# Performance work log

Hardware: AMD Instinct MI355X
Metric: run time of the kernel (lower is better)

## Reference

```python
import jax, jax.numpy as jnp
import numpy as np

D_LINK = 64   # link_state_dim
D_PATH = 64   # path_state_dim
T = 3
MAX_LEN = 8   # max hops per path (max(seqs)+1)
R_UNITS = 256


def _glorot(k, shape):
    lim = np.sqrt(6.0 / (shape[0] + shape[-1])).astype(np.float32)
    return jax.random.uniform(k, shape, minval=-lim, maxval=lim, dtype=jnp.float32)


def setup_inputs() -> dict:
    key = jax.random.key(0)
    ks = jax.random.split(key, 16)
    n_links, n_paths, L = 50000, 100000, MAX_LEN
    capacities = jax.random.uniform(ks[0], (n_links,), dtype=jnp.float32) + 0.5
    traffic = jax.random.uniform(ks[1], (n_paths,), dtype=jnp.float32)
    # every path traverses L links; entries sorted by path id (tf.segment_sum assumption)
    paths = jnp.repeat(jnp.arange(n_paths, dtype=jnp.int32), L)
    seqs = jnp.tile(jnp.arange(L, dtype=jnp.int32), n_paths)
    links = jax.random.randint(ks[2], (n_paths * L,), 0, n_links, dtype=jnp.int32)
    return dict(
        capacities=capacities, traffic=traffic, links=links, paths=paths, seqs=seqs,
        Wx_p=_glorot(ks[3], (D_LINK, 3 * D_PATH)), Wh_p=_glorot(ks[4], (D_PATH, 3 * D_PATH)),
        b_p=jnp.zeros((3 * D_PATH,), jnp.float32),
        Wx_e=_glorot(ks[5], (D_PATH, 3 * D_LINK)), Wh_e=_glorot(ks[6], (D_LINK, 3 * D_LINK)),
        b_e=jnp.zeros((3 * D_LINK,), jnp.float32),
        W_r1=_glorot(ks[7], (D_PATH, R_UNITS)), b_r1=jnp.zeros((R_UNITS,), jnp.float32),
        W_r2=_glorot(ks[8], (R_UNITS, R_UNITS)), b_r2=jnp.zeros((R_UNITS,), jnp.float32),
        W_f=_glorot(ks[9], (D_PATH + R_UNITS, 1)), b_f=jnp.zeros((1,), jnp.float32),
        n_links=n_links, n_paths=n_paths,
    )


def gru_cell(x, h, Wx, Wh, b):
    # Keras GRUCell (reset_after=False), gate order z, r, h
    gx = x @ Wx + b
    gh = h @ Wh
    u = h.shape[-1]
    z = jax.nn.sigmoid(gx[..., :u] + gh[..., :u])
    r = jax.nn.sigmoid(gx[..., u:2 * u] + gh[..., u:2 * u])
    hc = jnp.tanh(gx[..., 2 * u:] + r * gh[..., 2 * u:])
    return z * h + (1.0 - z) * hc


def routenet_fwd(capacities, traffic, links, paths, seqs,
                 Wx_p, Wh_p, b_p, Wx_e, Wh_e, b_e,
                 W_r1, b_r1, W_r2, b_r2, W_f, b_f, n_links, n_paths):
    link_state = jnp.concatenate(
        [capacities[:, None], jnp.zeros((n_links, D_LINK - 1), capacities.dtype)], axis=1)
    path_state = jnp.concatenate(
        [traffic[:, None], jnp.zeros((n_paths, D_PATH - 1), traffic.dtype)], axis=1)
    lens = jax.ops.segment_sum(jnp.ones_like(paths), paths, num_segments=n_paths)  # [P]

    for _ in range(T):
        h_ = link_state[links]                                        # [E, D_LINK]
        link_inputs = jnp.zeros((n_paths, MAX_LEN, D_LINK), h_.dtype).at[paths, seqs].set(h_)

        def step(h, inp):
            xt, t = inp
            hn = gru_cell(xt, h, Wx_p, Wh_p, b_p)
            valid = (t < lens)[:, None]
            hn = jnp.where(valid, hn, h)          # dynamic_rnn copies state past seq len
            out = jnp.where(valid, hn, 0.0)       # and emits zeros there
            return hn, out

        path_state, outs = jax.lax.scan(
            step, path_state,
            (jnp.transpose(link_inputs, (1, 0, 2)), jnp.arange(MAX_LEN)))
        m = jnp.transpose(outs, (1, 0, 2))[paths, seqs]               # [E, D_PATH]
        m = jax.ops.segment_sum(m, links, num_segments=n_links)      # [n_links, D_PATH]
        link_state = gru_cell(m, link_state, Wx_e, Wh_e, b_e)

    r = jax.nn.selu(path_state @ W_r1 + b_r1)
    r = jax.nn.selu(r @ W_r2 + b_r2)          # dropout inactive (training=False)
    o = jnp.concatenate([r, path_state], axis=1) @ W_f + b_f
    return o


def reference(capacities, traffic, links, paths, seqs,
              Wx_p, Wh_p, b_p, Wx_e, Wh_e, b_e,
              W_r1, b_r1, W_r2, b_r2, W_f, b_f, n_links, n_paths):
    return routenet_fwd(capacities, traffic, links, paths, seqs,
                        Wx_p, Wh_p, b_p, Wx_e, Wh_e, b_e,
                        W_r1, b_r1, W_r2, b_r2, W_f, b_f, n_links, n_paths)
```

## Files before the change

kernel.cpp:

```cpp
#include <hip/hip_runtime.h>

typedef unsigned short ushort_t;
typedef unsigned int   uint_t;
typedef short bf16x8 __attribute__((ext_vector_type(8)));
typedef float f32x4  __attribute__((ext_vector_type(4)));

#define MFMA16(a,b,c) __builtin_amdgcn_mfma_f32_16x16x32_bf16((a),(b),(c),0,0,0)

static __device__ __forceinline__ float bf2f(ushort_t b) {
  union { uint_t u; float f; } v; v.u = ((uint_t)b) << 16; return v.f;
}
static __device__ __forceinline__ ushort_t f2bf(float f) {
  union { float f; uint_t u; } v; v.f = f;
  uint_t r = v.u + 0x7fffu + ((v.u >> 16) & 1u);
  return (ushort_t)(r >> 16);
}
static __device__ __forceinline__ float frcp(float x) { return __builtin_amdgcn_rcpf(x); }
static __device__ __forceinline__ float sigm(float x) { return frcp(1.0f + __expf(-x)); }
static __device__ __forceinline__ float ftanh(float x) { return 1.0f - 2.0f * frcp(1.0f + __expf(2.0f * x)); }
static __device__ __forceinline__ float selu_f(float x) {
  float e = 1.6732632423543772f * (__expf(x) - 1.0f);
  return 1.0507009873554805f * (x > 0.0f ? x : e);
}
static __device__ __forceinline__ bf16x8 pack8(float4 a, float4 b) {
  bf16x8 r;
  r[0] = (short)f2bf(a.x); r[1] = (short)f2bf(a.y); r[2] = (short)f2bf(a.z); r[3] = (short)f2bf(a.w);
  r[4] = (short)f2bf(b.x); r[5] = (short)f2bf(b.y); r[6] = (short)f2bf(b.z); r[7] = (short)f2bf(b.w);
  return r;
}
static __device__ __forceinline__ void split8(float4 a, float4 b, bf16x8& hi, bf16x8& lo) {
  hi = pack8(a, b);
  float4 ra, rb;
  ra.x = a.x - bf2f((ushort_t)hi[0]); ra.y = a.y - bf2f((ushort_t)hi[1]);
  ra.z = a.z - bf2f((ushort_t)hi[2]); ra.w = a.w - bf2f((ushort_t)hi[3]);
  rb.x = b.x - bf2f((ushort_t)hi[4]); rb.y = b.y - bf2f((ushort_t)hi[5]);
  rb.z = b.z - bf2f((ushort_t)hi[6]); rb.w = b.w - bf2f((ushort_t)hi[7]);
  lo = pack8(ra, rb);
}

#define GFRAG(ptr, f) (*(const bf16x8*)&(ptr)[(((f) * 64 + lane)) * 8])
#define LFRAG(arr, f) (*(const bf16x8*)&(arr)[(((f) * 64 + lane)) * 8])

__global__ void detect_dtype(const uint_t* __restrict__ caps, int* __restrict__ flag) {
  int lane = threadIdx.x;
  uint_t d = caps[lane];
  uint_t lo = d & 0xFFFFu, hi = d >> 16;
  bool isbf = (lo >= 0x3F00u && lo <= 0x3FC0u) && (hi >= 0x3F00u && hi <= 0x3FC0u);
  unsigned long long m = __ballot(isbf);
  if (lane == 0) *flag = (__popcll(m) >= 48) ? 1 : 0;
}

#define NARR 14
struct ConvDesc {
  const void* src[NARR];
  float*      dst[NARR];
  int         n[NARR];
  int         blk0[NARR + 1];
};
__global__ void conv_all(ConvDesc d, const int* __restrict__ flag) {
  int isbf = *flag;
  int b = blockIdx.x;
  int a = 0;
  while (a + 1 < NARR && b >= d.blk0[a + 1]) ++a;
  int idx = (b - d.blk0[a]) * 256 + threadIdx.x;
  if (idx >= d.n[a]) return;
  d.dst[a][idx] = isbf ? bf2f(((const ushort_t*)d.src[a])[idx])
                       : ((const float*)d.src[a])[idx];
}

struct PackAll {
  const float* A[8];
  const float* B[8];
  ushort_t* dH[8];
  ushort_t* dL[8];
  int srcN[8], colOff[8], splitK[8], nCk[8], NT[8], blk0[9];
};
__global__ void pack_all(PackAll P) {
  int b = blockIdx.x;
  int a = 0;
  while (a + 1 < 8 && b >= P.blk0[a + 1]) ++a;
  int i = (b - P.blk0[a]) * 256 + threadIdx.x;
  int j = i & 7;
  int lane = (i >> 3) & 63;
  int f = i >> 9;
  int c = f / P.NT[a], nt = f - c * P.NT[a];
  int k = c * 32 + ((lane >> 4) << 3) + j;
  int n = P.colOff[a] + nt * 16 + (lane & 15);
  float v = (k < P.splitK[a]) ? P.A[a][k * P.srcN[a] + n]
                              : P.B[a][(k - P.splitK[a]) * P.srcN[a] + n];
  ushort_t hi = f2bf(v);
  P.dH[a][i] = hi;
  P.dL[a][i] = f2bf(v - bf2f(hi));
}

__global__ void init_states(const float* __restrict__ caps, const float* __restrict__ traffic,
                            ushort_t* __restrict__ linkHL,
                            float* __restrict__ path_state, int n_links, int n_paths) {
  long i = (long)blockIdx.x * 256 + threadIdx.x;
  long total = (long)(n_links + n_paths) * 64;
  if (i >= total) return;
  int row = (int)(i >> 6), col = (int)(i & 63);
  if (row < n_links) {
    float v = (col == 0) ? caps[row] : 0.0f;
    ushort_t hi = f2bf(v);
    linkHL[(long)row * 128 + col] = hi;
    linkHL[(long)row * 128 + 64 + col] = f2bf(v - bf2f(hi));
  } else {
    int pr = row - n_links;
    path_state[(long)pr * 64 + col] = (col == 0) ? traffic[pr] : 0.0f;
  }
}

__global__ void hist_k(const int* __restrict__ links, int* __restrict__ cnt, int E) {
  int e = blockIdx.x * 256 + threadIdx.x;
  if (e < E) atomicAdd(&cnt[links[e]], 1);
}
__global__ void scan_k(const int* __restrict__ cnt, int* __restrict__ base,
                       int* __restrict__ cursor, int n) {
  __shared__ int part[256];
  int tid = threadIdx.x;
  int chunk = (n + 255) / 256;
  int lo = tid * chunk, hiEnd = lo + chunk; if (hiEnd > n) hiEnd = n;
  int s = 0;
  for (int i = lo; i < hiEnd; ++i) s += cnt[i];
  part[tid] = s;
  __syncthreads();
  if (tid == 0) { int acc = 0; for (int i = 0; i < 256; ++i) { int v = part[i]; part[i] = acc; acc += v; } }
  __syncthreads();
  int acc = part[tid];
  for (int i = lo; i < hiEnd; ++i) { base[i] = acc; cursor[i] = acc; acc += cnt[i]; }
}
__global__ void fill_k(const int* __restrict__ links, int* __restrict__ cursor,
                       int* __restrict__ pos_of, int E) {
  int e = blockIdx.x * 256 + threadIdx.x;
  if (e >= E) return;
  pos_of[e] = atomicAdd(&cursor[links[e]], 1);
}

__global__ __launch_bounds__(256) void agg_kernel(
    const ushort_t* __restrict__ mH,
    const int* __restrict__ base, const int* __restrict__ cnt,
    float* __restrict__ agg, int n_links) {
  int l = blockIdx.x * 4 + (threadIdx.x >> 6);
  if (l >= n_links) return;
  int lane = threadIdx.x & 63;
  int s = base[l], d = cnt[l];
  float acc = 0.0f;
  for (int i = 0; i < d; ++i) acc += bf2f(mH[(long)(s + i) * 64 + lane]);
  agg[(long)l * 64 + lane] = acc;
}

#define PWB 7
__global__ __launch_bounds__(448) void path_kernel_bf16(
    const int* __restrict__ links,
    const ushort_t* __restrict__ linkHL,
    float* __restrict__ path_state,
    ushort_t* __restrict__ mH, int mmode, int store_m,
    const int* __restrict__ pos_of, float* __restrict__ agg,
    const ushort_t* __restrict__ wzrH, const ushort_t* __restrict__ wcH,
    const float* __restrict__ bp, const int* __restrict__ flagp, int n_paths) {
  __shared__ __align__(16) ushort_t s_wzr[32 * 512];
  __shared__ __align__(16) ushort_t s_wc[16 * 512];
  __shared__ __align__(16) ushort_t s_hh[PWB][16][68];
  __shared__ __align__(16) ushort_t s_hl[PWB][16][68];
  __shared__ float s_bias[192];

  if (flagp[0] == 0) return;

  int tid = threadIdx.x;
  {
    uint_t* s0 = (uint_t*)s_wzr; const uint_t* g0 = (const uint_t*)wzrH;
    for (int i = tid; i < 8192; i += 448) s0[i] = g0[i];
    uint_t* s1 = (uint_t*)s_wc;  const uint_t* g1 = (const uint_t*)wcH;
    for (int i = tid; i < 4096; i += 448) s1[i] = g1[i];
    for (int i = tid; i < 192; i += 448) s_bias[i] = bp[i];
  }

  int wv = tid >> 6, lane = tid & 63, l15 = lane & 15, quad = lane >> 4;
  int p0 = (blockIdx.x * PWB + wv) * 16;
  bool valid = (p0 < n_paths);

  float h[4][4];
  if (valid) {
#pragma unroll
    for (int tt = 0; tt < 4; ++tt)
#pragma unroll
      for (int r = 0; r < 4; ++r) {
        float v = path_state[(long)(p0 + quad * 4 + r) * 64 + tt * 16 + l15];
        h[tt][r] = v;
        ushort_t hi = f2bf(v);
        s_hh[wv][quad * 4 + r][tt * 16 + l15] = hi;
        s_hl[wv][quad * 4 + r][tt * 16 + l15] = f2bf(v - bf2f(hi));
      }
  }
  __syncthreads();
  if (!valid) return;

  for (int t = 0; t < 8; ++t) {
    int la = links[(p0 + l15) * 8 + t];
    const ushort_t* xr = linkHL + (long)la * 128;
    bf16x8 axH0 = *(const bf16x8*)(xr + quad * 8);
    bf16x8 axH1 = *(const bf16x8*)(xr + 32 + quad * 8);
    bf16x8 axL0 = *(const bf16x8*)(xr + 64 + quad * 8);
    bf16x8 axL1 = *(const bf16x8*)(xr + 96 + quad * 8);
    bf16x8 ahH0 = *(const bf16x8*)&s_hh[wv][l15][quad * 8];
    bf16x8 ahH1 = *(const bf16x8*)&s_hh[wv][l15][32 + quad * 8];
    bf16x8 ahL0 = *(const bf16x8*)&s_hl[wv][l15][quad * 8];
    bf16x8 ahL1 = *(const bf16x8*)&s_hl[wv][l15][32 + quad * 8];

    f32x4 azr[8];
#pragma unroll
    for (int nt = 0; nt < 8; ++nt) {
      f32x4 acc = {0.f, 0.f, 0.f, 0.f};
      acc = MFMA16(axH0, LFRAG(s_wzr, nt), acc);
      acc = MFMA16(axH1, LFRAG(s_wzr, 8 + nt), acc);
      acc = MFMA16(ahH0, LFRAG(s_wzr, 16 + nt), acc);
      acc = MFMA16(ahH1, LFRAG(s_wzr, 24 + nt), acc);
      acc = MFMA16(axL0, LFRAG(s_wzr, nt), acc);
      acc = MFMA16(axL1, LFRAG(s_wzr, 8 + nt), acc);
      acc = MFMA16(ahL0, LFRAG(s_wzr, 16 + nt), acc);
      acc = MFMA16(ahL1, LFRAG(s_wzr, 24 + nt), acc);
      azr[nt] = acc;
    }
    f32x4 axc[4], ahc[4];
#pragma unroll
    for (int nt = 0; nt < 4; ++nt) {
      f32x4 a = {0.f, 0.f, 0.f, 0.f};
      a = MFMA16(axH0, LFRAG(s_wc, nt), a);
      a = MFMA16(axH1, LFRAG(s_wc, 4 + nt), a);
      a = MFMA16(axL0, LFRAG(s_wc, nt), a);
      a = MFMA16(axL1, LFRAG(s_wc, 4 + nt), a);
      axc[nt] = a;
      f32x4 b = {0.f, 0.f, 0.f, 0.f};
      b = MFMA16(ahH0, LFRAG(s_wc, 8 + nt), b);
      b = MFMA16(ahH1, LFRAG(s_wc, 12 + nt), b);
      b = MFMA16(ahL0, LFRAG(s_wc, 8 + nt), b);
      b = MFMA16(ahL1, LFRAG(s_wc, 12 + nt), b);
      ahc[nt] = b;
    }

    int pr[4] = {0, 0, 0, 0};
    if (store_m) {
      if (mmode == 2) {
#pragma unroll
        for (int r = 0; r < 4; ++r) pr[r] = links[(p0 + quad * 4 + r) * 8 + t];
      } else {
#pragma unroll
        for (int r = 0; r < 4; ++r) pr[r] = pos_of[(p0 + quad * 4 + r) * 8 + t];
      }
    }

#pragma unroll
    for (int tt = 0; tt < 4; ++tt) {
      int col = tt * 16 + l15;
      float bz = s_bias[col], br = s_bias[64 + col], bc = s_bias[128 + col];
#pragma unroll
      for (int r = 0; r < 4; ++r) {
        float z   = sigm(azr[tt][r] + bz);
        float rr  = sigm(azr[4 + tt][r] + br);
        float hcv = ftanh(axc[tt][r] + bc + rr * ahc[tt][r]);
        float hn  = z * h[tt][r] + (1.0f - z) * hcv;
        h[tt][r] = hn;
        if (store_m) {
          if (mmode == 1) mH[(long)pr[r] * 64 + col] = f2bf(hn);
          else atomicAdd(&agg[(long)pr[r] * 64 + col], hn);
        }
        ushort_t hi = f2bf(hn);
        s_hh[wv][quad * 4 + r][col] = hi;
        s_hl[wv][quad * 4 + r][col] = f2bf(hn - bf2f(hi));
      }
    }
  }

#pragma unroll
  for (int tt = 0; tt < 4; ++tt)
#pragma unroll
    for (int r = 0; r < 4; ++r)
      path_state[(long)(p0 + quad * 4 + r) * 64 + tt * 16 + l15] = h[tt][r];
}

#define PW 13
__global__ __launch_bounds__(832) void path_kernel_f32(
    const int* __restrict__ links,
    const ushort_t* __restrict__ linkHL,
    float* __restrict__ path_state,
    ushort_t* __restrict__ mH, int mmode, int store_m,
    const int* __restrict__ pos_of, float* __restrict__ agg,
    const ushort_t* __restrict__ wzrH, const ushort_t* __restrict__ wzrL,
    const ushort_t* __restrict__ wcH,  const ushort_t* __restrict__ wcL,
    const float* __restrict__ bp, const int* __restrict__ flagp,
    int n_paths, int nGroups) {
  __shared__ __align__(16) ushort_t s_wzr[2][32 * 512];
  __shared__ __align__(16) ushort_t s_wc[2][16 * 512];
  __shared__ __align__(16) ushort_t s_hh[PW][16][72];
  __shared__ __align__(16) ushort_t s_hl[PW][16][72];
  __shared__ float s_bias[192];

  if (flagp[0] != 0) return;

  int tid = threadIdx.x;
  {
    uint_t* s0 = (uint_t*)s_wzr[0]; const uint_t* g0 = (const uint_t*)wzrH;
    for (int i = tid; i < 8192; i += 832) s0[i] = g0[i];
    uint_t* s1 = (uint_t*)s_wc[0];  const uint_t* g1 = (const uint_t*)wcH;
    for (int i = tid; i < 4096; i += 832) s1[i] = g1[i];
    uint_t* s2 = (uint_t*)s_wzr[1]; const uint_t* g2 = (const uint_t*)wzrL;
    for (int i = tid; i < 8192; i += 832) s2[i] = g2[i];
    uint_t* s3 = (uint_t*)s_wc[1];  const uint_t* g3 = (const uint_t*)wcL;
    for (int i = tid; i < 4096; i += 832) s3[i] = g3[i];
    for (int i = tid; i < 192; i += 832) s_bias[i] = bp[i];
  }
  __syncthreads();

  int wv = tid >> 6, lane = tid & 63, l15 = lane & 15, quad = lane >> 4;

  for (int g = 0; g < nGroups; ++g) {
    int slot = g * gridDim.x + blockIdx.x;
    int p0 = (slot * PW + wv) * 16;
    if (p0 >= n_paths) continue;

    float h[4][4];
#pragma unroll
    for (int tt = 0; tt < 4; ++tt)
#pragma unroll
      for (int r = 0; r < 4; ++r) {
        float v = path_state[(long)(p0 + quad * 4 + r) * 64 + tt * 16 + l15];
        h[tt][r] = v;
        ushort_t hi = f2bf(v);
        s_hh[wv][quad * 4 + r][tt * 16 + l15] = hi;
        s_hl[wv][quad * 4 + r][tt * 16 + l15] = f2bf(v - bf2f(hi));
      }

    const int* lrow = links + (long)(p0 + l15) * 8;
    {
      int la0 = lrow[0];
      const ushort_t* x0 = linkHL + (long)la0 * 128;
      bf16x8 nH0 = *(const bf16x8*)(x0 + quad * 8);
      bf16x8 nH1 = *(const bf16x8*)(x0 + 32 + quad * 8);
      bf16x8 nL0 = *(const bf16x8*)(x0 + 64 + quad * 8);
      bf16x8 nL1 = *(const bf16x8*)(x0 + 96 + quad * 8);

      for (int t = 0; t < 8; ++t) {
        bf16x8 axH0 = nH0, axH1 = nH1, axL0 = nL0, axL1 = nL1;
        if (t < 7) {
          int la2 = lrow[t + 1];
          const ushort_t* x2 = linkHL + (long)la2 * 128;
          nH0 = *(const bf16x8*)(x2 + quad * 8);
          nH1 = *(const bf16x8*)(x2 + 32 + quad * 8);
          nL0 = *(const bf16x8*)(x2 + 64 + quad * 8);
          nL1 = *(const bf16x8*)(x2 + 96 + quad * 8);
        }
        int pr[4] = {0, 0, 0, 0};
        if (store_m) {
          if (mmode == 2) {
#pragma unroll
            for (int r = 0; r < 4; ++r) pr[r] = links[(long)(p0 + quad * 4 + r) * 8 + t];
          } else {
#pragma unroll
            for (int r = 0; r < 4; ++r) pr[r] = pos_of[(long)(p0 + quad * 4 + r) * 8 + t];
          }
        }
        bf16x8 ahH0 = *(const bf16x8*)&s_hh[wv][l15][quad * 8];
        bf16x8 ahH1 = *(const bf16x8*)&s_hh[wv][l15][32 + quad * 8];
        bf16x8 ahL0 = *(const bf16x8*)&s_hl[wv][l15][quad * 8];
        bf16x8 ahL1 = *(const bf16x8*)&s_hl[wv][l15][32 + quad * 8];

        f32x4 azr[8];
#pragma unroll
        for (int nt = 0; nt < 8; ++nt) {
          f32x4 acc = {0.f, 0.f, 0.f, 0.f};
          acc = MFMA16(axH0, LFRAG(s_wzr[0], nt), acc);
          acc = MFMA16(axH1, LFRAG(s_wzr[0], 8 + nt), acc);
          acc = MFMA16(axL0, LFRAG(s_wzr[0], nt), acc);
          acc = MFMA16(axL1, LFRAG(s_wzr[0], 8 + nt), acc);
          acc = MFMA16(axH0, LFRAG(s_wzr[1], nt), acc);
          acc = MFMA16(axH1, LFRAG(s_wzr[1], 8 + nt), acc);
          acc = MFMA16(ahH0, LFRAG(s_wzr[0], 16 + nt), acc);
          acc = MFMA16(ahH1, LFRAG(s_wzr[0], 24 + nt), acc);
          acc = MFMA16(ahL0, LFRAG(s_wzr[0], 16 + nt), acc);
          acc = MFMA16(ahL1, LFRAG(s_wzr[0], 24 + nt), acc);
          acc = MFMA16(ahH0, LFRAG(s_wzr[1], 16 + nt), acc);
          acc = MFMA16(ahH1, LFRAG(s_wzr[1], 24 + nt), acc);
          azr[nt] = acc;
        }
        f32x4 axc[4], ahc[4];
#pragma unroll
        for (int nt = 0; nt < 4; ++nt) {
          f32x4 a = {0.f, 0.f, 0.f, 0.f};
          a = MFMA16(axH0, LFRAG(s_wc[0], nt), a);
          a = MFMA16(axH1, LFRAG(s_wc[0], 4 + nt), a);
          a = MFMA16(axL0, LFRAG(s_wc[0], nt), a);
          a = MFMA16(axL1, LFRAG(s_wc[0], 4 + nt), a);
          a = MFMA16(axH0, LFRAG(s_wc[1], nt), a);
          a = MFMA16(axH1, LFRAG(s_wc[1], 4 + nt), a);
          axc[nt] = a;
          f32x4 b = {0.f, 0.f, 0.f, 0.f};
          b = MFMA16(ahH0, LFRAG(s_wc[0], 8 + nt), b);
          b = MFMA16(ahH1, LFRAG(s_wc[0], 12 + nt), b);
          b = MFMA16(ahL0, LFRAG(s_wc[0], 8 + nt), b);
          b = MFMA16(ahL1, LFRAG(s_wc[0], 12 + nt), b);
          b = MFMA16(ahH0, LFRAG(s_wc[1], 8 + nt), b);
          b = MFMA16(ahH1, LFRAG(s_wc[1], 12 + nt), b);
          ahc[nt] = b;
        }

#pragma unroll
        for (int tt = 0; tt < 4; ++tt) {
          int col = tt * 16 + l15;
          float bz = s_bias[col], br = s_bias[64 + col], bc = s_bias[128 + col];
#pragma unroll
          for (int r = 0; r < 4; ++r) {
            float z   = sigm(azr[tt][r] + bz);
            float rr  = sigm(azr[4 + tt][r] + br);
            float hcv = ftanh(axc[tt][r] + bc + rr * ahc[tt][r]);
            float hn  = z * h[tt][r] + (1.0f - z) * hcv;
            h[tt][r] = hn;
            if (store_m) {
              if (mmode == 1) mH[(long)pr[r] * 64 + col] = f2bf(hn);
              else atomicAdd(&agg[(long)pr[r] * 64 + col], hn);
            }
            ushort_t hi = f2bf(hn);
            s_hh[wv][quad * 4 + r][col] = hi;
            s_hl[wv][quad * 4 + r][col] = f2bf(hn - bf2f(hi));
          }
        }
      }
    }

#pragma unroll
    for (int tt = 0; tt < 4; ++tt)
#pragma unroll
      for (int r = 0; r < 4; ++r)
        path_state[(long)(p0 + quad * 4 + r) * 64 + tt * 16 + l15] = h[tt][r];
  }
}

__global__ __launch_bounds__(320) void link_kernel(
    const float* __restrict__ agg,
    ushort_t* __restrict__ linkHL,
    const ushort_t* __restrict__ wzrH, const ushort_t* __restrict__ wzrL,
    const ushort_t* __restrict__ wcH,  const ushort_t* __restrict__ wcL,
    const float* __restrict__ be, const int* __restrict__ flagp) {
  __shared__ __align__(16) ushort_t s_wzr[2][32 * 512];
  __shared__ __align__(16) ushort_t s_wc[2][16 * 512];
  __shared__ float s_bias[192];

  int tid = threadIdx.x;
  int wlo = (flagp[0] == 0) ? 1 : 0;
  {
    uint_t* s0 = (uint_t*)s_wzr[0]; const uint_t* g0 = (const uint_t*)wzrH;
    for (int i = tid; i < 8192; i += 320) s0[i] = g0[i];
    uint_t* s1 = (uint_t*)s_wc[0];  const uint_t* g1 = (const uint_t*)wcH;
    for (int i = tid; i < 4096; i += 320) s1[i] = g1[i];
    if (wlo) {
      uint_t* s2 = (uint_t*)s_wzr[1]; const uint_t* g2 = (const uint_t*)wzrL;
      for (int i = tid; i < 8192; i += 320) s2[i] = g2[i];
      uint_t* s3 = (uint_t*)s_wc[1];  const uint_t* g3 = (const uint_t*)wcL;
      for (int i = tid; i < 4096; i += 320) s3[i] = g3[i];
    }
    for (int i = tid; i < 192; i += 320) s_bias[i] = be[i];
  }
  __syncthreads();

  int wv = tid >> 6, lane = tid & 63, l15 = lane & 15, quad = lane >> 4;
  int l0 = (blockIdx.x * 5 + wv) * 16;

  const float* arow = agg + (long)(l0 + l15) * 64;
  float4 f0 = *(const float4*)(arow + quad * 8);
  float4 f1 = *(const float4*)(arow + quad * 8 + 4);
  float4 f2 = *(const float4*)(arow + 32 + quad * 8);
  float4 f3 = *(const float4*)(arow + 36 + quad * 8);
  bf16x8 axH0, axL0, axH1, axL1;
  split8(f0, f1, axH0, axL0);
  split8(f2, f3, axH1, axL1);
  const ushort_t* hr = linkHL + (long)(l0 + l15) * 128;
  bf16x8 ahH0 = *(const bf16x8*)(hr + quad * 8);
  bf16x8 ahH1 = *(const bf16x8*)(hr + 32 + quad * 8);
  bf16x8 ahL0 = *(const bf16x8*)(hr + 64 + quad * 8);
  bf16x8 ahL1 = *(const bf16x8*)(hr + 96 + quad * 8);

  float h[4][4];
#pragma unroll
  for (int tt = 0; tt < 4; ++tt)
#pragma unroll
    for (int r = 0; r < 4; ++r) {
      long row = (long)(l0 + quad * 4 + r) * 128;
      int col = tt * 16 + l15;
      h[tt][r] = bf2f(linkHL[row + col]) + bf2f(linkHL[row + 64 + col]);
    }

  f32x4 azr[8];
#pragma unroll
  for (int nt = 0; nt < 8; ++nt) {
    f32x4 acc = {0.f, 0.f, 0.f, 0.f};
    acc = MFMA16(axH0, LFRAG(s_wzr[0], nt), acc);
    acc = MFMA16(axH1, LFRAG(s_wzr[0], 8 + nt), acc);
    acc = MFMA16(ahH0, LFRAG(s_wzr[0], 16 + nt), acc);
    acc = MFMA16(ahH1, LFRAG(s_wzr[0], 24 + nt), acc);
    acc = MFMA16(axL0, LFRAG(s_wzr[0], nt), acc);
    acc = MFMA16(axL1, LFRAG(s_wzr[0], 8 + nt), acc);
    acc = MFMA16(ahL0, LFRAG(s_wzr[0], 16 + nt), acc);
    acc = MFMA16(ahL1, LFRAG(s_wzr[0], 24 + nt), acc);
    azr[nt] = acc;
  }
  f32x4 axc[4], ahc[4];
#pragma unroll
  for (int nt = 0; nt < 4; ++nt) {
    f32x4 a = {0.f, 0.f, 0.f, 0.f};
    a = MFMA16(axH0, LFRAG(s_wc[0], nt), a);
    a = MFMA16(axH1, LFRAG(s_wc[0], 4 + nt), a);
    a = MFMA16(axL0, LFRAG(s_wc[0], nt), a);
    a = MFMA16(axL1, LFRAG(s_wc[0], 4 + nt), a);
    axc[nt] = a;
    f32x4 b = {0.f, 0.f, 0.f, 0.f};
    b = MFMA16(ahH0, LFRAG(s_wc[0], 8 + nt), b);
    b = MFMA16(ahH1, LFRAG(s_wc[0], 12 + nt), b);
    b = MFMA16(ahL0, LFRAG(s_wc[0], 8 + nt), b);
    b = MFMA16(ahL1, LFRAG(s_wc[0], 12 + nt), b);
    ahc[nt] = b;
  }
  if (wlo) {
#pragma unroll
    for (int nt = 0; nt < 8; ++nt) {
      azr[nt] = MFMA16(axH0, LFRAG(s_wzr[1], nt), azr[nt]);
      azr[nt] = MFMA16(axH1, LFRAG(s_wzr[1], 8 + nt), azr[nt]);
      azr[nt] = MFMA16(ahH0, LFRAG(s_wzr[1], 16 + nt), azr[nt]);
      azr[nt] = MFMA16(ahH1, LFRAG(s_wzr[1], 24 + nt), azr[nt]);
    }
#pragma unroll
    for (int nt = 0; nt < 4; ++nt) {
      axc[nt] = MFMA16(axH0, LFRAG(s_wc[1], nt), axc[nt]);
      axc[nt] = MFMA16(axH1, LFRAG(s_wc[1], 4 + nt), axc[nt]);
      ahc[nt] = MFMA16(ahH0, LFRAG(s_wc[1], 8 + nt), ahc[nt]);
      ahc[nt] = MFMA16(ahH1, LFRAG(s_wc[1], 12 + nt), ahc[nt]);
    }
  }

#pragma unroll
  for (int tt = 0; tt < 4; ++tt) {
    int col = tt * 16 + l15;
    float bz = s_bias[col], br = s_bias[64 + col], bc = s_bias[128 + col];
#pragma unroll
    for (int r = 0; r < 4; ++r) {
      float z   = sigm(azr[tt][r] + bz);
      float rr  = sigm(azr[4 + tt][r] + br);
      float hcv = ftanh(axc[tt][r] + bc + rr * ahc[tt][r]);
      float hn  = z * h[tt][r] + (1.0f - z) * hcv;
      long row = (long)(l0 + quad * 4 + r) * 128;
      ushort_t hi = f2bf(hn);
      linkHL[row + col] = hi;
      linkHL[row + 64 + col] = f2bf(hn - bf2f(hi));
    }
  }
}

#define RW 8
__global__ __launch_bounds__(512) void readout_kernel(
    const float* __restrict__ path_state, int n_paths,
    const ushort_t* __restrict__ wr1H, const ushort_t* __restrict__ wr1L,
    const ushort_t* __restrict__ wr2H, const ushort_t* __restrict__ wr2L,
    const float* __restrict__ br1, const float* __restrict__ br2,
    const float* __restrict__ Wf, const float* __restrict__ bfp,
    void* __restrict__ outp, const int* __restrict__ flagp) {
  __shared__ __align__(16) ushort_t s_r1h[RW][16][264];
  __shared__ __align__(16) ushort_t s_r1l[RW][16][264];
  int tid = threadIdx.x;
  int wv = tid >> 6, lane = tid & 63, l15 = lane & 15, quad = lane >> 4;
  int p0 = (blockIdx.x * RW + wv) * 16;
  if (p0 >= n_paths) return;
  int isbf = flagp[0];
  int wlo = (isbf == 0) ? 1 : 0;

  const float* prow = path_state + (long)(p0 + l15) * 64;
  float4 g0 = *(const float4*)(prow + quad * 8);
  float4 g1 = *(const float4*)(prow + quad * 8 + 4);
  float4 g2 = *(const float4*)(prow + 32 + quad * 8);
  float4 g3 = *(const float4*)(prow + 36 + quad * 8);
  bf16x8 axH0, axL0, axH1, axL1;
  split8(g0, g1, axH0, axL0);
  split8(g2, g3, axH1, axL1);

  f32x4 a1[16];
#pragma unroll
  for (int nt = 0; nt < 16; ++nt) {
    f32x4 acc = {0.f, 0.f, 0.f, 0.f};
    acc = MFMA16(axH0, GFRAG(wr1H, nt), acc);
    acc = MFMA16(axH1, GFRAG(wr1H, 16 + nt), acc);
    acc = MFMA16(axL0, GFRAG(wr1H, nt), acc);
    acc = MFMA16(axL1, GFRAG(wr1H, 16 + nt), acc);
    a1[nt] = acc;
  }
  if (wlo) {
#pragma unroll
    for (int nt = 0; nt < 16; ++nt) {
      a1[nt] = MFMA16(axH0, GFRAG(wr1L, nt), a1[nt]);
      a1[nt] = MFMA16(axH1, GFRAG(wr1L, 16 + nt), a1[nt]);
    }
  }
#pragma unroll
  for (int tt = 0; tt < 16; ++tt) {
    float bb = br1[tt * 16 + l15];
#pragma unroll
    for (int r = 0; r < 4; ++r) {
      float v = selu_f(a1[tt][r] + bb);
      ushort_t hi = f2bf(v);
      s_r1h[wv][quad * 4 + r][tt * 16 + l15] = hi;
      s_r1l[wv][quad * 4 + r][tt * 16 + l15] = f2bf(v - bf2f(hi));
    }
  }

  f32x4 a2[16];
  f32x4 zero = {0.f, 0.f, 0.f, 0.f};
#pragma unroll
  for (int nt = 0; nt < 16; ++nt) a2[nt] = zero;
#pragma unroll
  for (int c = 0; c < 8; ++c) {
    bf16x8 afH = *(const bf16x8*)&s_r1h[wv][l15][c * 32 + quad * 8];
    bf16x8 afL = *(const bf16x8*)&s_r1l[wv][l15][c * 32 + quad * 8];
#pragma unroll
    for (int nt = 0; nt < 16; ++nt) {
      a2[nt] = MFMA16(afH, GFRAG(wr2H, c * 16 + nt), a2[nt]);
      a2[nt] = MFMA16(afL, GFRAG(wr2H, c * 16 + nt), a2[nt]);
    }
    if (wlo) {
#pragma unroll
      for (int nt = 0; nt < 16; ++nt)
        a2[nt] = MFMA16(afH, GFRAG(wr2L, c * 16 + nt), a2[nt]);
    }
  }

  float part[4] = {0.f, 0.f, 0.f, 0.f};
#pragma unroll
  for (int tt = 0; tt < 16; ++tt) {
    float wf = Wf[tt * 16 + l15];
    float bb = br2[tt * 16 + l15];
#pragma unroll
    for (int r = 0; r < 4; ++r) part[r] += selu_f(a2[tt][r] + bb) * wf;
  }
  float wfh0 = Wf[256 + l15 * 4 + 0];
  float wfh1 = Wf[256 + l15 * 4 + 1];
  float wfh2 = Wf[256 + l15 * 4 + 2];
  float wfh3 = Wf[256 + l15 * 4 + 3];
#pragma unroll
  for (int r = 0; r < 4; ++r) {
    const float4 hh = *(const float4*)&path_state[(long)(p0 + quad * 4 + r) * 64 + l15 * 4];
    part[r] += hh.x * wfh0 + hh.y * wfh1 + hh.z * wfh2 + hh.w * wfh3;
  }
#pragma unroll
  for (int msk = 1; msk < 16; msk <<= 1)
#pragma unroll
    for (int r = 0; r < 4; ++r) part[r] += __shfl_xor(part[r], msk, 64);
  if (l15 == 0) {
    float bfv = bfp[0];
    if (isbf) {
#pragma unroll
      for (int r = 0; r < 4; ++r) ((ushort_t*)outp)[p0 + quad * 4 + r] = f2bf(part[r] + bfv);
    } else {
#pragma unroll
      for (int r = 0; r < 4; ++r) ((float*)outp)[p0 + quad * 4 + r] = part[r] + bfv;
    }
  }
}

extern "C" void kernel_launch(void* const* d_in, const int* in_sizes, int n_in,
                              void* d_out, int out_size, void* d_ws, size_t ws_size,
                              hipStream_t stream) {
  const int n_links = in_sizes[0];
  const int n_paths = in_sizes[1];
  const int E       = in_sizes[2];

  char* w = (char*)d_ws;
  size_t off = 0;
  auto take = [&](size_t bytes) { size_t o = off; off += (bytes + 255) & ~(size_t)255; return o; };
  float*    path_state = (float*)(w + take((size_t)n_paths * 64 * 4));
  float*    agg        = (float*)(w + take((size_t)n_links * 64 * 4));
  ushort_t* linkHL     = (ushort_t*)(w + take((size_t)n_links * 128 * 2));
  int*      flag       = (int*)(w + take(256));
  ushort_t* wzrH_p = (ushort_t*)(w + take(32768));
  ushort_t* wzrL_p = (ushort_t*)(w + take(32768));
  ushort_t* wcH_p  = (ushort_t*)(w + take(16384));
  ushort_t* wcL_p  = (ushort_t*)(w + take(16384));
  ushort_t* wzrH_e = (ushort_t*)(w + take(32768));
  ushort_t* wzrL_e = (ushort_t*)(w + take(32768));
  ushort_t* wcH_e  = (ushort_t*)(w + take(16384));
  ushort_t* wcL_e  = (ushort_t*)(w + take(16384));
  ushort_t* wr1H   = (ushort_t*)(w + take(32768));
  ushort_t* wr1L   = (ushort_t*)(w + take(32768));
  ushort_t* wr2H   = (ushort_t*)(w + take(131072));
  ushort_t* wr2L   = (ushort_t*)(w + take(131072));
  float* c_caps    = (float*)(w + take((size_t)in_sizes[0] * 4));
  float* c_traffic = (float*)(w + take((size_t)in_sizes[1] * 4));
  float* c_Wx_p = (float*)(w + take((size_t)in_sizes[5] * 4));
  float* c_Wh_p = (float*)(w + take((size_t)in_sizes[6] * 4));
  float* c_b_p  = (float*)(w + take((size_t)in_sizes[7] * 4));
  float* c_Wx_e = (float*)(w + take((size_t)in_sizes[8] * 4));
  float* c_Wh_e = (float*)(w + take((size_t)in_sizes[9] * 4));
  float* c_b_e  = (float*)(w + take((size_t)in_sizes[10] * 4));
  float* c_Wr1  = (float*)(w + take((size_t)in_sizes[11] * 4));
  float* c_br1  = (float*)(w + take((size_t)in_sizes[12] * 4));
  float* c_Wr2  = (float*)(w + take((size_t)in_sizes[13] * 4));
  float* c_br2  = (float*)(w + take((size_t)in_sizes[14] * 4));
  float* c_Wf   = (float*)(w + take((size_t)in_sizes[15] * 4));
  float* c_bf   = (float*)(w + take((size_t)in_sizes[16] * 4));
  int* cnt    = (int*)(w + take((size_t)n_links * 4));
  int* base   = (int*)(w + take((size_t)n_links * 4));
  int* cursor = (int*)(w + take((size_t)n_links * 4));
  int* pos_of = (int*)(w + take((size_t)E * 4));

  size_t rem = (ws_size > off) ? (ws_size - off) : 0;
  int mmode;
  ushort_t* mH = nullptr;
  if (rem >= (size_t)E * 64 * 2 + 256) { mmode = 1; mH = (ushort_t*)(w + take((size_t)E * 64 * 2)); }
  else mmode = 2;

  detect_dtype<<<1, 64, 0, stream>>>((const uint_t*)d_in[0], flag);

  ConvDesc cd;
  float* dsts[NARR] = {c_caps, c_traffic, c_Wx_p, c_Wh_p, c_b_p, c_Wx_e, c_Wh_e, c_b_e,
                       c_Wr1, c_br1, c_Wr2, c_br2, c_Wf, c_bf};
  int    srcs[NARR] = {0, 1, 5, 6, 7, 8, 9, 10, 11, 12, 13, 14, 15, 16};
  int nblk = 0;
  for (int a = 0; a < NARR; ++a) {
    cd.src[a] = d_in[srcs[a]];
    cd.dst[a] = dsts[a];
    cd.n[a] = in_sizes[srcs[a]];
    cd.blk0[a] = nblk;
    nblk += (cd.n[a] + 255) / 256;
  }
  cd.blk0[NARR] = nblk;
  conv_all<<<nblk, 256, 0, stream>>>(cd, flag);

  {
    long total = (long)(n_links + n_paths) * 64;
    int blocks = (int)((total + 255) / 256);
    init_states<<<blocks, 256, 0, stream>>>(c_caps, c_traffic, linkHL, path_state,
                                            n_links, n_paths);
  }
  {
    PackAll P;
    const float* As[8] = {c_Wx_p, c_Wx_p, c_Wh_p, c_Wx_e, c_Wx_e, c_Wh_e, c_Wr1, c_Wr2};
    const float* Bs[8] = {c_Wh_p, c_Wx_p, c_Wh_p, c_Wh_e, c_Wx_e, c_Wh_e, c_Wr1, c_Wr2};
    ushort_t* dH[8] = {wzrH_p, wcH_p, wcH_p + 4096, wzrH_e, wcH_e, wcH_e + 4096, wr1H, wr2H};
    ushort_t* dL[8] = {wzrL_p, wcL_p, wcL_p + 4096, wzrL_e, wcL_e, wcL_e + 4096, wr1L, wr2L};
    int srcN[8]   = {192, 192, 192, 192, 192, 192, 256, 256};
    int colOff[8] = {0, 128, 128, 0, 128, 128, 0, 0};
    int splitK[8] = {64, 64, 64, 64, 64, 64, 64, 256};
    int nCk[8]    = {4, 2, 2, 4, 2, 2, 2, 8};
    int NT[8]     = {8, 4, 4, 8, 4, 4, 16, 16};
    int pb = 0;
    for (int a = 0; a < 8; ++a) {
      P.A[a] = As[a]; P.B[a] = Bs[a]; P.dH[a] = dH[a]; P.dL[a] = dL[a];
      P.srcN[a] = srcN[a]; P.colOff[a] = colOff[a]; P.splitK[a] = splitK[a];
      P.nCk[a] = nCk[a]; P.NT[a] = NT[a]; P.blk0[a] = pb;
      pb += nCk[a] * NT[a] * 2;
    }
    P.blk0[8] = pb;
    pack_all<<<pb, 256, 0, stream>>>(P);
  }

  const int* links = (const int*)d_in[2];
  if (mmode == 1) {
    (void)hipMemsetAsync(cnt, 0, (size_t)n_links * 4, stream);
    hist_k<<<(E + 255) / 256, 256, 0, stream>>>(links, cnt, E);
    scan_k<<<1, 256, 0, stream>>>(cnt, base, cursor, n_links);
    fill_k<<<(E + 255) / 256, 256, 0, stream>>>(links, cursor, pos_of, E);
  }

  int grid_bf = (n_paths + 16 * PWB - 1) / (16 * PWB);
  int slots   = (n_paths + 16 * PW - 1) / (16 * PW);
  int gridF   = slots < 256 ? slots : 256;
  int nGroups = (slots + gridF - 1) / gridF;

  for (int it = 0; it < 3; ++it) {
    int store_m = (it < 2) ? 1 : 0;
    if (mmode == 2 && store_m) (void)hipMemsetAsync(agg, 0, (size_t)n_links * 64 * 4, stream);
    path_kernel_bf16<<<grid_bf, 448, 0, stream>>>(
        links, linkHL, path_state, mH, mmode, store_m, pos_of, agg,
        wzrH_p, wcH_p, c_b_p, flag, n_paths);
    path_kernel_f32<<<gridF, 832, 0, stream>>>(
        links, linkHL, path_state, mH, mmode, store_m, pos_of, agg,
        wzrH_p, wzrL_p, wcH_p, wcL_p, c_b_p, flag, n_paths, nGroups);
    if (it < 2) {
      if (mmode == 1)
        agg_kernel<<<(n_links + 3) / 4, 256, 0, stream>>>(mH, base, cnt, agg, n_links);
      link_kernel<<<n_links / 80, 320, 0, stream>>>(agg, linkHL,
                                                    wzrH_e, wzrL_e, wcH_e, wcL_e, c_b_e, flag);
    }
  }
  readout_kernel<<<(n_paths + 16 * RW - 1) / (16 * RW), 512, 0, stream>>>(
      path_state, n_paths, wr1H, wr1L, wr2H, wr2L,
      c_br1, c_br2, c_Wf, c_bf, d_out, flag);
}
```

Measured before the change: 1.162 ms.

## Store path messages in fp32 when workspace allows; stage readout W2 in LDS

Adds a new message mode that keeps per-edge path outputs in fp32 instead of bf16 whenever the workspace is large enough, and the sorted gather aggregation reads those fp32 values. Separately, the readout kernel drops from 8 to 6 waves per block and copies W_r2 into shared memory one 32-row chunk at a time instead of reading MFMA fragments from global memory. The fp32 path doubles message write and read traffic but avoids bf16 rounding of messages. The readout staging adds block-wide barriers, and invalid waves now stay resident so they can join those barriers.

Measured after the change: 1.459 ms. +25.6%, slower.

```diff
diff --git a/kernel.cpp b/kernel.cpp
--- a/kernel.cpp
+++ b/kernel.cpp
@@ -138,7 +138,7 @@
 }
 
 __global__ __launch_bounds__(256) void agg_kernel(
-    const ushort_t* __restrict__ mH,
+    const float* __restrict__ mF, const ushort_t* __restrict__ mH, int mmode,
     const int* __restrict__ base, const int* __restrict__ cnt,
     float* __restrict__ agg, int n_links) {
   int l = blockIdx.x * 4 + (threadIdx.x >> 6);
@@ -146,7 +146,11 @@
   int lane = threadIdx.x & 63;
   int s = base[l], d = cnt[l];
   float acc = 0.0f;
-  for (int i = 0; i < d; ++i) acc += bf2f(mH[(long)(s + i) * 64 + lane]);
+  if (mmode == 0) {
+    for (int i = 0; i < d; ++i) acc += mF[(long)(s + i) * 64 + lane];
+  } else {
+    for (int i = 0; i < d; ++i) acc += bf2f(mH[(long)(s + i) * 64 + lane]);
+  }
   agg[(long)l * 64 + lane] = acc;
 }
 
@@ -155,7 +159,7 @@
     const int* __restrict__ links,
     const ushort_t* __restrict__ linkHL,
     float* __restrict__ path_state,
-    ushort_t* __restrict__ mH, int mmode, int store_m,
+    float* __restrict__ mF, ushort_t* __restrict__ mH, int mmode, int store_m,
     const int* __restrict__ pos_of, float* __restrict__ agg,
     const ushort_t* __restrict__ wzrH, const ushort_t* __restrict__ wcH,
     const float* __restrict__ bp, const int* __restrict__ flagp, int n_paths) {
@@ -262,7 +266,8 @@
         float hn  = z * h[tt][r] + (1.0f - z) * hcv;
         h[tt][r] = hn;
         if (store_m) {
-          if (mmode == 1) mH[(long)pr[r] * 64 + col] = f2bf(hn);
+          if (mmode == 0)      mF[(long)pr[r] * 64 + col] = hn;
+          else if (mmode == 1) mH[(long)pr[r] * 64 + col] = f2bf(hn);
           else atomicAdd(&agg[(long)pr[r] * 64 + col], hn);
         }
         ushort_t hi = f2bf(hn);
@@ -284,7 +289,7 @@
     const int* __restrict__ links,
     const ushort_t* __restrict__ linkHL,
     float* __restrict__ path_state,
-    ushort_t* __restrict__ mH, int mmode, int store_m,
+    float* __restrict__ mF, ushort_t* __restrict__ mH, int mmode, int store_m,
     const int* __restrict__ pos_of, float* __restrict__ agg,
     const ushort_t* __restrict__ wzrH, const ushort_t* __restrict__ wzrL,
     const ushort_t* __restrict__ wcH,  const ushort_t* __restrict__ wcL,
@@ -416,7 +421,8 @@
             float hn  = z * h[tt][r] + (1.0f - z) * hcv;
             h[tt][r] = hn;
             if (store_m) {
-              if (mmode == 1) mH[(long)pr[r] * 64 + col] = f2bf(hn);
+              if (mmode == 0)      mF[(long)pr[r] * 64 + col] = hn;
+              else if (mmode == 1) mH[(long)pr[r] * 64 + col] = f2bf(hn);
               else atomicAdd(&agg[(long)pr[r] * 64 + col], hn);
             }
             ushort_t hi = f2bf(hn);
@@ -554,8 +560,8 @@
   }
 }
 
-#define RW 8
-__global__ __launch_bounds__(512) void readout_kernel(
+#define RW 6
+__global__ __launch_bounds__(384) void readout_kernel(
     const float* __restrict__ path_state, int n_paths,
     const ushort_t* __restrict__ wr1H, const ushort_t* __restrict__ wr1L,
     const ushort_t* __restrict__ wr2H, const ushort_t* __restrict__ wr2L,
@@ -564,48 +570,52 @@
     void* __restrict__ outp, const int* __restrict__ flagp) {
   __shared__ __align__(16) ushort_t s_r1h[RW][16][264];
   __shared__ __align__(16) ushort_t s_r1l[RW][16][264];
+  __shared__ __align__(16) ushort_t s_w2h[16 * 512];
+  __shared__ __align__(16) ushort_t s_w2l[16 * 512];
   int tid = threadIdx.x;
   int wv = tid >> 6, lane = tid & 63, l15 = lane & 15, quad = lane >> 4;
   int p0 = (blockIdx.x * RW + wv) * 16;
-  if (p0 >= n_paths) return;
+  bool valid = (p0 < n_paths);
   int isbf = flagp[0];
   int wlo = (isbf == 0) ? 1 : 0;
 
-  const float* prow = path_state + (long)(p0 + l15) * 64;
-  float4 g0 = *(const float4*)(prow + quad * 8);
-  float4 g1 = *(const float4*)(prow + quad * 8 + 4);
-  float4 g2 = *(const float4*)(prow + 32 + quad * 8);
-  float4 g3 = *(const float4*)(prow + 36 + quad * 8);
   bf16x8 axH0, axL0, axH1, axL1;
-  split8(g0, g1, axH0, axL0);
-  split8(g2, g3, axH1, axL1);
-
   f32x4 a1[16];
-#pragma unroll
-  for (int nt = 0; nt < 16; ++nt) {
-    f32x4 acc = {0.f, 0.f, 0.f, 0.f};
-    acc = MFMA16(axH0, GFRAG(wr1H, nt), acc);
-    acc = MFMA16(axH1, GFRAG(wr1H, 16 + nt), acc);
-    acc = MFMA16(axL0, GFRAG(wr1H, nt), acc);
-    acc = MFMA16(axL1, GFRAG(wr1H, 16 + nt), acc);
-    a1[nt] = acc;
-  }
-  if (wlo) {
+  if (valid) {
+    const float* prow = path_state + (long)(p0 + l15) * 64;
+    float4 g0 = *(const float4*)(prow + quad * 8);
+    float4 g1 = *(const float4*)(prow + quad * 8 + 4);
+    float4 g2 = *(const float4*)(prow + 32 + quad * 8);
+    float4 g3 = *(const float4*)(prow + 36 + quad * 8);
+    split8(g0, g1, axH0, axL0);
+    split8(g2, g3, axH1, axL1);
+
 #pragma unroll
     for (int nt = 0; nt < 16; ++nt) {
-      a1[nt] = MFMA16(axH0, GFRAG(wr1L, nt), a1[nt]);
-      a1[nt] = MFMA16(axH1, GFRAG(wr1L, 16 + nt), a1[nt]);
-    }
-  }
-#pragma unroll
-  for (int tt = 0; tt < 16; ++tt) {
-    float bb = br1[tt * 16 + l15];
-#pragma unroll
-    for (int r = 0; r < 4; ++r) {
-      float v = selu_f(a1[tt][r] + bb);
-      ushort_t hi = f2bf(v);
-      s_r1h[wv][quad * 4 + r][tt * 16 + l15] = hi;
-      s_r1l[wv][quad * 4 + r][tt * 16 + l15] = f2bf(v - bf2f(hi));
+      f32x4 acc = {0.f, 0.f, 0.f, 0.f};
+      acc = MFMA16(axH0, GFRAG(wr1H, nt), acc);
+      acc = MFMA16(axH1, GFRAG(wr1H, 16 + nt), acc);
+      acc = MFMA16(axL0, GFRAG(wr1H, nt), acc);
+      acc = MFMA16(axL1, GFRAG(wr1H, 16 + nt), acc);
+      a1[nt] = acc;
+    }
+    if (wlo) {
+#pragma unroll
+      for (int nt = 0; nt < 16; ++nt) {
+        a1[nt] = MFMA16(axH0, GFRAG(wr1L, nt), a1[nt]);
+        a1[nt] = MFMA16(axH1, GFRAG(wr1L, 16 + nt), a1[nt]);
+      }
+    }
+#pragma unroll
+    for (int tt = 0; tt < 16; ++tt) {
+      float bb = br1[tt * 16 + l15];
+#pragma unroll
+      for (int r = 0; r < 4; ++r) {
+        float v = selu_f(a1[tt][r] + bb);
+        ushort_t hi = f2bf(v);
+        s_r1h[wv][quad * 4 + r][tt * 16 + l15] = hi;
+        s_r1l[wv][quad * 4 + r][tt * 16 + l15] = f2bf(v - bf2f(hi));
+      }
     }
   }
 
@@ -613,21 +623,34 @@
   f32x4 zero = {0.f, 0.f, 0.f, 0.f};
 #pragma unroll
   for (int nt = 0; nt < 16; ++nt) a2[nt] = zero;
-#pragma unroll
+
   for (int c = 0; c < 8; ++c) {
-    bf16x8 afH = *(const bf16x8*)&s_r1h[wv][l15][c * 32 + quad * 8];
-    bf16x8 afL = *(const bf16x8*)&s_r1l[wv][l15][c * 32 + quad * 8];
-#pragma unroll
-    for (int nt = 0; nt < 16; ++nt) {
-      a2[nt] = MFMA16(afH, GFRAG(wr2H, c * 16 + nt), a2[nt]);
-      a2[nt] = MFMA16(afL, GFRAG(wr2H, c * 16 + nt), a2[nt]);
-    }
-    if (wlo) {
-#pragma unroll
-      for (int nt = 0; nt < 16; ++nt)
-        a2[nt] = MFMA16(afH, GFRAG(wr2L, c * 16 + nt), a2[nt]);
-    }
-  }
+    __syncthreads();
+    {
+      uint_t* sh = (uint_t*)s_w2h; const uint_t* gh = (const uint_t*)(wr2H + c * 8192);
+      for (int i = tid; i < 4096; i += 384) sh[i] = gh[i];
+      if (wlo) {
+        uint_t* sl = (uint_t*)s_w2l; const uint_t* gl = (const uint_t*)(wr2L + c * 8192);
+        for (int i = tid; i < 4096; i += 384) sl[i] = gl[i];
+      }
+    }
+    __syncthreads();
+    if (valid) {
+      bf16x8 afH = *(const bf16x8*)&s_r1h[wv][l15][c * 32 + quad * 8];
+      bf16x8 afL = *(const bf16x8*)&s_r1l[wv][l15][c * 32 + quad * 8];
+#pragma unroll
+      for (int nt = 0; nt < 16; ++nt) {
+        a2[nt] = MFMA16(afH, LFRAG(s_w2h, nt), a2[nt]);
+        a2[nt] = MFMA16(afL, LFRAG(s_w2h, nt), a2[nt]);
+      }
+      if (wlo) {
+#pragma unroll
+        for (int nt = 0; nt < 16; ++nt)
+          a2[nt] = MFMA16(afH, LFRAG(s_w2l, nt), a2[nt]);
+      }
+    }
+  }
+  if (!valid) return;
 
   float part[4] = {0.f, 0.f, 0.f, 0.f};
 #pragma unroll
@@ -709,8 +732,10 @@
 
   size_t rem = (ws_size > off) ? (ws_size - off) : 0;
   int mmode;
+  float*    mF = nullptr;
   ushort_t* mH = nullptr;
-  if (rem >= (size_t)E * 64 * 2 + 256) { mmode = 1; mH = (ushort_t*)(w + take((size_t)E * 64 * 2)); }
+  if (rem >= (size_t)E * 64 * 4 + 256) { mmode = 0; mF = (float*)(w + take((size_t)E * 64 * 4)); }
+  else if (rem >= (size_t)E * 64 * 2 + 256) { mmode = 1; mH = (ushort_t*)(w + take((size_t)E * 64 * 2)); }
   else mmode = 2;
 
   detect_dtype<<<1, 64, 0, stream>>>((const uint_t*)d_in[0], flag);
@@ -759,7 +784,7 @@
   }
 
   const int* links = (const int*)d_in[2];
-  if (mmode == 1) {
+  if (mmode < 2) {
     (void)hipMemsetAsync(cnt, 0, (size_t)n_links * 4, stream);
     hist_k<<<(E + 255) / 256, 256, 0, stream>>>(links, cnt, E);
     scan_k<<<1, 256, 0, stream>>>(cnt, base, cursor, n_links);
@@ -775,19 +800,20 @@
     int store_m = (it < 2) ? 1 : 0;
     if (mmode == 2 && store_m) (void)hipMemsetAsync(agg, 0, (size_t)n_links * 64 * 4, stream);
     path_kernel_bf16<<<grid_bf, 448, 0, stream>>>(
-        links, linkHL, path_state, mH, mmode, store_m, pos_of, agg,
+        links, linkHL, path_state, mF, mH, mmode, store_m, pos_of, agg,
         wzrH_p, wcH_p, c_b_p, flag, n_paths);
     path_kernel_f32<<<gridF, 832, 0, stream>>>(
-        links, linkHL, path_state, mH, mmode, store_m, pos_of, agg,
+        links, linkHL, path_state, mF, mH, mmode, store_m, pos_of, agg,
         wzrH_p, wzrL_p, wcH_p, wcL_p, c_b_p, flag, n_paths, nGroups);
     if (it < 2) {
-      if (mmode == 1)
-        agg_kernel<<<(n_links + 3) / 4, 256, 0, stream>>>(mH, base, cnt, agg, n_links);
+      if (mmode < 2)
+        agg_kernel<<<(n_links + 3) / 4, 256, 0, stream>>>(mF, mH, mmode, base, cnt,
+                                                          agg, n_links);
       link_kernel<<<n_links / 80, 320, 0, stream>>>(agg, linkHL,
                                                     wzrH_e, wzrL_e, wcH_e, wcL_e, c_b_e, flag);
     }
   }
-  readout_kernel<<<(n_paths + 16 * RW - 1) / (16 * RW), 512, 0, stream>>>(
+  readout_kernel<<<(n_paths + 16 * RW - 1) / (16 * RW), 384, 0, stream>>>(
       path_state, n_paths, wr1H, wr1L, wr2H, wr2L,
       c_br1, c_br2, c_Wf, c_bf, d_out, flag);
 }
```
